# Kernel optimization log

Measured on AMD Instinct MI355X. Metric: run time of the kernel, lower is better.

The kernel has to match this reference:

```python
import jax, jax.numpy as jnp
import numpy as np

EMBED_DIM = 256
HIDDEN_DIM = 128
NUM_VARS = 1024


def _linear_params(key, fan_in, fan_out):
    kw, kb = jax.random.split(key)
    lim = 1.0 / np.sqrt(fan_in)
    W = jax.random.uniform(kw, (fan_in, fan_out), minval=-lim, maxval=lim, dtype=jnp.float32)
    b = jax.random.uniform(kb, (fan_out,), minval=-lim, maxval=lim, dtype=jnp.float32)
    return W, b


def setup_inputs() -> dict:
    key = jax.random.key(0)
    ks = jax.random.split(key, 7)
    next_state_embedding = jax.random.normal(ks[0], (EMBED_DIM,), dtype=jnp.float32)
    prev_variable_embeddings = jax.random.normal(ks[1], (NUM_VARS, EMBED_DIM), dtype=jnp.float32)
    Wq, bq = _linear_params(ks[2], EMBED_DIM, HIDDEN_DIM)
    Wk, bk = _linear_params(ks[3], EMBED_DIM, HIDDEN_DIM)
    Wc, bc = _linear_params(ks[4], EMBED_DIM, HIDDEN_DIM)
    W1, b1 = _linear_params(ks[5], 2 * HIDDEN_DIM, HIDDEN_DIM)
    W2, b2 = _linear_params(ks[6], HIDDEN_DIM, 1)
    return {
        "next_state_embedding": next_state_embedding,
        "prev_variable_embeddings": prev_variable_embeddings,
        "Wq": Wq, "bq": bq,
        "Wk": Wk, "bk": bk,
        "Wc": Wc, "bc": bc,
        "W1": W1, "b1": b1,
        "W2": W2, "b2": b2,
    }


def reference(next_state_embedding, prev_variable_embeddings,
              Wq, bq, Wk, bk, Wc, bc, W1, b1, W2, b2):
    n = prev_variable_embeddings.shape[0]
    h = Wq.shape[1]
    # context_net: Linear + ReLU on next-state embedding -> [h]
    context = jax.nn.relu(next_state_embedding @ Wc + bc)
    # queries/keys over prev vars, each shifted by context -> [n, h]
    queries = prev_variable_embeddings @ Wq + bq + context
    keys = prev_variable_embeddings @ Wk + bk + context
    # pair_scorer layer 1 on concat(q_i, k_j) decomposes:
    # hidden[i,j] = relu(q_i @ W1[:h] + k_j @ W1[h:] + b1)
    q_proj = queries @ W1[:h]            # [n, h]
    k_proj = keys @ W1[h:]               # [n, h]
    hidden = jax.nn.relu(q_proj[:, None, :] + k_proj[None, :, :] + b1)  # [n, n, h]
    scores = jnp.squeeze(hidden @ W2, axis=-1) + b2[0]  # [n, n]
    # extract i < j pairs in row-major order (matches the nested loop)
    iu, ju = jnp.triu_indices(n, k=1)
    return scores[iu, ju]  # [n*(n-1)/2]
```

## Files before the change

### kernel.cpp

```cpp
#include <hip/hip_runtime.h>

#define N 1024
#define E 256
#define H 128

__global__ void ctx_kernel(const float* __restrict__ x, const float* __restrict__ Wc,
                           const float* __restrict__ bc, float* __restrict__ ctx) {
    int h = threadIdx.x;
    float acc = bc[h];
    for (int e = 0; e < E; ++e) acc += x[e] * Wc[e * H + h];
    ctx[h] = fmaxf(acc, 0.f);
}

__global__ void proj_kernel(const float* __restrict__ P,
                            const float* __restrict__ Wq, const float* __restrict__ bq,
                            const float* __restrict__ Wk, const float* __restrict__ bk,
                            const float* __restrict__ W1, const float* __restrict__ b1,
                            const float* __restrict__ ctx,
                            float* __restrict__ qp, float* __restrict__ kp) {
    __shared__ float prow[E];
    __shared__ float qrow[H];
    __shared__ float krow[H];
    int i = blockIdx.x;
    int h = threadIdx.x;
    prow[h]     = P[i * E + h];
    prow[h + H] = P[i * E + h + H];
    __syncthreads();
    float c = ctx[h];
    float sq = bq[h] + c;
    float sk = bk[h] + c;
    for (int e = 0; e < E; ++e) {
        float p = prow[e];
        sq += p * Wq[e * H + h];
        sk += p * Wk[e * H + h];
    }
    qrow[h] = sq;
    krow[h] = sk;
    __syncthreads();
    float aq = b1[h];
    float ak = 0.f;
    for (int r = 0; r < H; ++r) {
        aq += qrow[r] * W1[r * H + h];
        ak += krow[r] * W1[(H + r) * H + h];
    }
    qp[i * H + h] = aq;
    kp[i * H + h] = ak;
}

__global__ __launch_bounds__(256) void pair_kernel(
    const float* __restrict__ qp, const float* __restrict__ kp,
    const float* __restrict__ W2, const float* __restrict__ b2,
    float* __restrict__ out) {
    int bi = blockIdx.y, bj = blockIdx.x;
    if (bj < bi) return;

    __shared__ __align__(16) float qs[32][132];
    __shared__ __align__(16) float ks[32][132];
    __shared__ __align__(16) float w2s[H];

    int t = threadIdx.x;
    if (t < H) w2s[t] = W2[t];

    const float4* qp4 = (const float4*)(qp + bi * 32 * H);
    const float4* kp4 = (const float4*)(kp + bj * 32 * H);
#pragma unroll
    for (int v = 0; v < 4; ++v) {
        int idx = v * 256 + t;
        int r = idx >> 5, c = idx & 31;
        float4 q = qp4[r * 32 + c];
        float4 k = kp4[r * 32 + c];
        *((float4*)&qs[r][c * 4]) = q;
        *((float4*)&ks[r][c * 4]) = k;
    }
    __syncthreads();

    int tj  = t & 31;
    int ti0 = t >> 5;
    float b2v = b2[0];
    float acc[4];
#pragma unroll
    for (int u = 0; u < 4; ++u) acc[u] = b2v;

    const float4* ksr = (const float4*)&ks[tj][0];
    const float4* w24 = (const float4*)&w2s[0];
    for (int h4 = 0; h4 < 32; ++h4) {
        float4 k4 = ksr[h4];
        float4 w4 = w24[h4];
#pragma unroll
        for (int u = 0; u < 4; ++u) {
            const float4 q4 = *((const float4*)&qs[ti0 + u * 8][h4 * 4]);
            acc[u] += fmaxf(q4.x + k4.x, 0.f) * w4.x;
            acc[u] += fmaxf(q4.y + k4.y, 0.f) * w4.y;
            acc[u] += fmaxf(q4.z + k4.z, 0.f) * w4.z;
            acc[u] += fmaxf(q4.w + k4.w, 0.f) * w4.w;
        }
    }

#pragma unroll
    for (int u = 0; u < 4; ++u) {
        int i = bi * 32 + ti0 + u * 8;
        int j = bj * 32 + tj;
        if (j > i) {
            int base = i * (2 * N - i - 1) / 2;
            out[base + (j - i - 1)] = acc[u];
        }
    }
}

extern "C" void kernel_launch(void* const* d_in, const int* in_sizes, int n_in,
                              void* d_out, int out_size, void* d_ws, size_t ws_size,
                              hipStream_t stream) {
    const float* x  = (const float*)d_in[0];
    const float* P  = (const float*)d_in[1];
    const float* Wq = (const float*)d_in[2];
    const float* bq = (const float*)d_in[3];
    const float* Wk = (const float*)d_in[4];
    const float* bk = (const float*)d_in[5];
    const float* Wc = (const float*)d_in[6];
    const float* bc = (const float*)d_in[7];
    const float* W1 = (const float*)d_in[8];
    const float* b1 = (const float*)d_in[9];
    const float* W2 = (const float*)d_in[10];
    const float* b2 = (const float*)d_in[11];
    float* out = (float*)d_out;

    float* ws  = (float*)d_ws;
    float* ctx = ws;
    float* qp  = ws + 128;
    float* kp  = qp + N * H;

    ctx_kernel<<<1, 128, 0, stream>>>(x, Wc, bc, ctx);
    proj_kernel<<<N, 128, 0, stream>>>(P, Wq, bq, Wk, bk, W1, b1, ctx, qp, kp);
    dim3 grid(32, 32);
    pair_kernel<<<grid, 256, 0, stream>>>(qp, kp, W2, b2, out);
}
```

Baseline: 114.7 us.

## Fold W1 into projection weights and compute pair scores in fp16 with dot2

Precomputes Wq·W1a and Wk·W1b plus constant bias vectors in a setup kernel, so the projection kernel does one GEMV-like pass over four rows per block and writes fp16 q/k. The pair kernel stores q/k/W2 in half, uses packed half add/relu and fdot2 accumulation, and widens tiles to 32x64 to reuse q across more keys. The aim is to cut ALU work and shared memory traffic in the dominant n² stage. The cost is reduced precision in the hidden activations, which risks tolerance failures.

```diff
diff --git a/kernel.cpp b/kernel.cpp
--- a/kernel.cpp
+++ b/kernel.cpp
@@ -4,105 +4,191 @@
 #define E 256
 #define H 128
 
-__global__ void ctx_kernel(const float* __restrict__ x, const float* __restrict__ Wc,
-                           const float* __restrict__ bc, float* __restrict__ ctx) {
-    int h = threadIdx.x;
-    float acc = bc[h];
-    for (int e = 0; e < E; ++e) acc += x[e] * Wc[e * H + h];
-    ctx[h] = fmaxf(acc, 0.f);
-}
-
-__global__ void proj_kernel(const float* __restrict__ P,
-                            const float* __restrict__ Wq, const float* __restrict__ bq,
-                            const float* __restrict__ Wk, const float* __restrict__ bk,
-                            const float* __restrict__ W1, const float* __restrict__ b1,
-                            const float* __restrict__ ctx,
-                            float* __restrict__ qp, float* __restrict__ kp) {
-    __shared__ float prow[E];
-    __shared__ float qrow[H];
-    __shared__ float krow[H];
-    int i = blockIdx.x;
-    int h = threadIdx.x;
-    prow[h]     = P[i * E + h];
-    prow[h + H] = P[i * E + h + H];
+typedef _Float16 hv2 __attribute__((ext_vector_type(2)));
+typedef _Float16 half_t;
+
+__device__ __forceinline__ float dot2_acc(hv2 a, hv2 b, float c) {
+#if __has_builtin(__builtin_amdgcn_fdot2)
+    return __builtin_amdgcn_fdot2(a, b, c, false);
+#else
+    return c + (float)a.x * (float)b.x + (float)a.y * (float)b.y;
+#endif
+}
+
+__device__ __forceinline__ hv2 relu_add2(hv2 a, hv2 b) {
+    hv2 s = a + b;
+    hv2 z = (hv2)(_Float16)0.f;
+    return __builtin_elementwise_max(s, z);
+}
+
+__global__ __launch_bounds__(256) void setup_kernel(
+    const float* __restrict__ x, const float* __restrict__ Wc, const float* __restrict__ bc,
+    const float* __restrict__ Wq, const float* __restrict__ bq,
+    const float* __restrict__ Wk, const float* __restrict__ bk,
+    const float* __restrict__ W1, const float* __restrict__ b1,
+    float* __restrict__ Wqp, float* __restrict__ Wkp,
+    float* __restrict__ constq, float* __restrict__ constk) {
+    int b = blockIdx.x;
+    int t = threadIdx.x;
+    if (b < E) {
+        __shared__ float wq_s[H], wk_s[H];
+        if (t < H) wq_s[t] = Wq[b * H + t];
+        else       wk_s[t - H] = Wk[b * H + (t - H)];
+        __syncthreads();
+        int h = t & (H - 1);
+        float acc = 0.f;
+        if (t < H) {
+#pragma unroll 8
+            for (int r = 0; r < H; ++r) acc += wq_s[r] * W1[r * H + h];
+            Wqp[b * H + h] = acc;
+        } else {
+#pragma unroll 8
+            for (int r = 0; r < H; ++r) acc += wk_s[r] * W1[(H + r) * H + h];
+            Wkp[b * H + h] = acc;
+        }
+    } else {
+        __shared__ float xs[E];
+        __shared__ float pc[2][H];
+        __shared__ float aq_s[H], ak_s[H];
+        xs[t] = x[t];
+        __syncthreads();
+        int h = t & (H - 1);
+        int c = t >> 7;
+        float p = 0.f;
+#pragma unroll 8
+        for (int e = c * H; e < c * H + H; ++e) p += xs[e] * Wc[e * H + h];
+        pc[c][h] = p;
+        __syncthreads();
+        if (t < H) {
+            float ctxv = fmaxf(pc[0][t] + pc[1][t] + bc[t], 0.f);
+            aq_s[t] = bq[t] + ctxv;
+            ak_s[t] = bk[t] + ctxv;
+        }
+        __syncthreads();
+        float acc;
+        if (t < H) {
+            acc = b1[h];
+#pragma unroll 8
+            for (int r = 0; r < H; ++r) acc += aq_s[r] * W1[r * H + h];
+            constq[h] = acc;
+        } else {
+            acc = 0.f;
+#pragma unroll 8
+            for (int r = 0; r < H; ++r) acc += ak_s[r] * W1[(H + r) * H + h];
+            constk[h] = acc;
+        }
+    }
+}
+
+__global__ __launch_bounds__(256) void proj_kernel(
+    const float* __restrict__ P,
+    const float* __restrict__ Wqp, const float* __restrict__ Wkp,
+    const float* __restrict__ constq, const float* __restrict__ constk,
+    half_t* __restrict__ qh, half_t* __restrict__ kh) {
+    __shared__ __align__(16) float p_s[4 * E];
+    int b = blockIdx.x;
+    int i0 = b * 4;
+    int t = threadIdx.x;
+    ((float4*)p_s)[t] = ((const float4*)(P + i0 * E))[t];
     __syncthreads();
-    float c = ctx[h];
-    float sq = bq[h] + c;
-    float sk = bk[h] + c;
-    for (int e = 0; e < E; ++e) {
-        float p = prow[e];
-        sq += p * Wq[e * H + h];
-        sk += p * Wk[e * H + h];
-    }
-    qrow[h] = sq;
-    krow[h] = sk;
-    __syncthreads();
-    float aq = b1[h];
-    float ak = 0.f;
-    for (int r = 0; r < H; ++r) {
-        aq += qrow[r] * W1[r * H + h];
-        ak += krow[r] * W1[(H + r) * H + h];
-    }
-    qp[i * H + h] = aq;
-    kp[i * H + h] = ak;
-}
-
+    bool isq = t < H;
+    int h = t & (H - 1);
+    const float* M = isq ? Wqp : Wkp;
+    float cv = isq ? constq[h] : constk[h];
+    float a0 = cv, a1 = cv, a2 = cv, a3 = cv;
+    for (int e = 0; e < E; e += 4) {
+        float4 p0 = *(const float4*)&p_s[0 * E + e];
+        float4 p1 = *(const float4*)&p_s[1 * E + e];
+        float4 p2 = *(const float4*)&p_s[2 * E + e];
+        float4 p3 = *(const float4*)&p_s[3 * E + e];
+        float m0 = M[(e + 0) * H + h];
+        float m1 = M[(e + 1) * H + h];
+        float m2 = M[(e + 2) * H + h];
+        float m3 = M[(e + 3) * H + h];
+        a0 += p0.x * m0 + p0.y * m1 + p0.z * m2 + p0.w * m3;
+        a1 += p1.x * m0 + p1.y * m1 + p1.z * m2 + p1.w * m3;
+        a2 += p2.x * m0 + p2.y * m1 + p2.z * m2 + p2.w * m3;
+        a3 += p3.x * m0 + p3.y * m1 + p3.z * m2 + p3.w * m3;
+    }
+    half_t* O = isq ? qh : kh;
+    O[(i0 + 0) * H + h] = (half_t)a0;
+    O[(i0 + 1) * H + h] = (half_t)a1;
+    O[(i0 + 2) * H + h] = (half_t)a2;
+    O[(i0 + 3) * H + h] = (half_t)a3;
+}
+
+#define QSTR 136
 __global__ __launch_bounds__(256) void pair_kernel(
-    const float* __restrict__ qp, const float* __restrict__ kp,
+    const half_t* __restrict__ qh, const half_t* __restrict__ kh,
     const float* __restrict__ W2, const float* __restrict__ b2,
     float* __restrict__ out) {
-    int bi = blockIdx.y, bj = blockIdx.x;
-    if (bj < bi) return;
-
-    __shared__ __align__(16) float qs[32][132];
-    __shared__ __align__(16) float ks[32][132];
-    __shared__ __align__(16) float w2s[H];
+    int bj = blockIdx.x;
+    int bi = blockIdx.y;
+    if (bj * 64 + 63 <= bi * 32) return;
+
+    __shared__ __align__(16) half_t qs[32][QSTR];
+    __shared__ __align__(16) half_t ks[64][QSTR];
+    __shared__ __align__(16) half_t w2s[H];
 
     int t = threadIdx.x;
-    if (t < H) w2s[t] = W2[t];
-
-    const float4* qp4 = (const float4*)(qp + bi * 32 * H);
-    const float4* kp4 = (const float4*)(kp + bj * 32 * H);
+    if (t < H) w2s[t] = (half_t)W2[t];
+
+    const float4* qh4 = (const float4*)(qh + bi * 32 * H);
+    const float4* kh4 = (const float4*)(kh + bj * 64 * H);
+#pragma unroll
+    for (int v = 0; v < 2; ++v) {
+        int idx = v * 256 + t;
+        int r = idx >> 4, c = idx & 15;
+        float4 q = qh4[idx];
+        *(float4*)&qs[r][c * 8] = q;
+    }
 #pragma unroll
     for (int v = 0; v < 4; ++v) {
         int idx = v * 256 + t;
-        int r = idx >> 5, c = idx & 31;
-        float4 q = qp4[r * 32 + c];
-        float4 k = kp4[r * 32 + c];
-        *((float4*)&qs[r][c * 4]) = q;
-        *((float4*)&ks[r][c * 4]) = k;
+        int r = idx >> 4, c = idx & 15;
+        float4 k = kh4[idx];
+        *(float4*)&ks[r][c * 8] = k;
     }
     __syncthreads();
 
-    int tj  = t & 31;
+    int jj  = t & 31;
     int ti0 = t >> 5;
     float b2v = b2[0];
-    float acc[4];
-#pragma unroll
-    for (int u = 0; u < 4; ++u) acc[u] = b2v;
-
-    const float4* ksr = (const float4*)&ks[tj][0];
-    const float4* w24 = (const float4*)&w2s[0];
-    for (int h4 = 0; h4 < 32; ++h4) {
-        float4 k4 = ksr[h4];
-        float4 w4 = w24[h4];
+    float acc[4][2];
+#pragma unroll
+    for (int u = 0; u < 4; ++u) { acc[u][0] = b2v; acc[u][1] = b2v; }
+
+    for (int h8 = 0; h8 < 16; ++h8) {
+        float4 wf = *(const float4*)&w2s[h8 * 8];
+        float4 ka = *(const float4*)&ks[jj][h8 * 8];
+        float4 kb = *(const float4*)&ks[jj + 32][h8 * 8];
+        const hv2* wp  = (const hv2*)&wf;
+        const hv2* kap = (const hv2*)&ka;
+        const hv2* kbp = (const hv2*)&kb;
 #pragma unroll
         for (int u = 0; u < 4; ++u) {
-            const float4 q4 = *((const float4*)&qs[ti0 + u * 8][h4 * 4]);
-            acc[u] += fmaxf(q4.x + k4.x, 0.f) * w4.x;
-            acc[u] += fmaxf(q4.y + k4.y, 0.f) * w4.y;
-            acc[u] += fmaxf(q4.z + k4.z, 0.f) * w4.z;
-            acc[u] += fmaxf(q4.w + k4.w, 0.f) * w4.w;
+            float4 qf = *(const float4*)&qs[ti0 + u * 8][h8 * 8];
+            const hv2* qp2 = (const hv2*)&qf;
+#pragma unroll
+            for (int s = 0; s < 4; ++s) {
+                hv2 sa = relu_add2(qp2[s], kap[s]);
+                hv2 sb = relu_add2(qp2[s], kbp[s]);
+                acc[u][0] = dot2_acc(sa, wp[s], acc[u][0]);
+                acc[u][1] = dot2_acc(sb, wp[s], acc[u][1]);
+            }
         }
     }
 
 #pragma unroll
     for (int u = 0; u < 4; ++u) {
         int i = bi * 32 + ti0 + u * 8;
-        int j = bj * 32 + tj;
-        if (j > i) {
-            int base = i * (2 * N - i - 1) / 2;
-            out[base + (j - i - 1)] = acc[u];
+#pragma unroll
+        for (int jv = 0; jv < 2; ++jv) {
+            int j = bj * 64 + jj + jv * 32;
+            if (j > i) {
+                int base = i * (2 * N - i - 1) / 2;
+                out[base + (j - i - 1)] = acc[u][jv];
+            }
         }
     }
 }
@@ -124,13 +210,17 @@
     const float* b2 = (const float*)d_in[11];
     float* out = (float*)d_out;
 
-    float* ws  = (float*)d_ws;
-    float* ctx = ws;
-    float* qp  = ws + 128;
-    float* kp  = qp + N * H;
-
-    ctx_kernel<<<1, 128, 0, stream>>>(x, Wc, bc, ctx);
-    proj_kernel<<<N, 128, 0, stream>>>(P, Wq, bq, Wk, bk, W1, b1, ctx, qp, kp);
-    dim3 grid(32, 32);
-    pair_kernel<<<grid, 256, 0, stream>>>(qp, kp, W2, b2, out);
-}
+    float* ws     = (float*)d_ws;
+    float* constq = ws;
+    float* constk = ws + H;
+    float* Wqp    = ws + 2 * H;
+    float* Wkp    = Wqp + E * H;
+    half_t* qh    = (half_t*)(Wkp + E * H);
+    half_t* kh    = qh + N * H;
+
+    setup_kernel<<<E + 1, 256, 0, stream>>>(x, Wc, bc, Wq, bq, Wk, bk, W1, b1,
+                                            Wqp, Wkp, constq, constk);
+    proj_kernel<<<N / 4, 256, 0, stream>>>(P, Wqp, Wkp, constq, constk, qh, kh);
+    dim3 grid(16, 32);
+    pair_kernel<<<grid, 256, 0, stream>>>(qh, kh, W2, b2, out);
+}
```

Result: faster. 103.8 us (-9.6%).
